# Kernel optimization log

Hardware: AMD Instinct MI355X
Metric: run time of the kernel (lower is better)

## Reference

```python
import jax, jax.numpy as jnp
import numpy as np

N_ROUTINGS = 3


def squash(v, axis=-1):
    sn = jnp.sum(jnp.square(v), axis=axis, keepdims=True)
    return (jnp.sqrt(sn) / (1.0 + sn)) * v


def setup_inputs() -> dict:
    key = jax.random.key(0)
    k1, k2 = jax.random.split(key)
    B, R, C, n_in, d_in = 16, 14, 14, 64, 16
    n_caps, caps_dim = 10, 16
    inputs = jax.random.normal(k1, (B, R, C, n_in, d_in), dtype=jnp.float32)
    W = jax.random.normal(k2, (n_caps, n_in, d_in, caps_dim), dtype=jnp.float32) * 0.1
    return {"inputs": inputs, "W": W}


def reference(inputs, W):
    # inputs: [B,R,C,i,e], W: [n,i,e,o] -> res (u_hat): [B,R,C,n,i,o]
    res = jnp.einsum('brcie,nieo->brcnio', inputs, W)
    n_in = inputs.shape[3]
    # softmax of zeros over last axis -> uniform 1/n_in
    b = jnp.full(res.shape[:-1], 1.0 / n_in, dtype=res.dtype)  # [B,R,C,n,i]
    for _ in range(N_ROUTINGS - 1):
        v = squash(jnp.sum(b[..., None] * res, axis=-2))  # [B,R,C,n,o]
        b = b + jnp.sum(res * v[..., None, :], axis=-1)   # agreement
    out = squash(jnp.sum(b[..., None] * res, axis=-2))
    return out  # [B,R,C,n_caps,caps_dim]
```

## Files before the change

kernel.cpp:

```cpp
#include <hip/hip_runtime.h>
#include <hip/hip_bf16.h>

typedef __attribute__((ext_vector_type(4))) float f32x4;
typedef __attribute__((ext_vector_type(8))) short s16x8;

#define QPB 4


template<int CTRL>
__device__ __forceinline__ float dpp_add(float x) {
    int v = __builtin_amdgcn_update_dpp(0, __float_as_int(x), CTRL, 0xF, 0xF, true);
    return x + __int_as_float(v);
}
template<int CTRL>
__device__ __forceinline__ float dpp_movf(float x) {
    return __int_as_float(__builtin_amdgcn_update_dpp(0, __float_as_int(x), CTRL, 0xF, 0xF, true));
}

__global__ __launch_bounds__(256, 4) void caps_kernel(
    const float* __restrict__ inp,
    const float* __restrict__ W,
    float* __restrict__ out)
{
    const int tid = threadIdx.x;
    const int w   = tid >> 6;
    const int l   = tid & 63;
    const int n   = blockIdx.x / 196;
    const int qg  = blockIdx.x % 196;
    const int q0  = qg * QPB;

    extern __shared__ __align__(16) char smem[];
    char* res_s = smem;

    const int i4 = l >> 2;
    const int oq = l & 3;
    const int i_ = w * 16 + i4;
    const int col = l & 15;
    const int kg  = l >> 4;

    const float* wb = W + (size_t)n * 16384 + i_ * 256 + oq * 4;
    f32x4 wrot[16];
#pragma unroll
    for (int r = 0; r < 4; ++r) {
        int c = (oq + r) & 3;
#pragma unroll
        for (int kk = 0; kk < 4; ++kk)
            wrot[r * 4 + kk] = *(const f32x4*)(wb + (c * 4 + kk) * 16);
    }

    s16x8 ones;
#pragma unroll
    for (int j = 0; j < 8; ++j) ones[j] = (short)0x3F80;

    for (int t = 0; t < QPB; ++t) {
        const int q = q0 + t;
        char* rbuf = res_s + (t & 1) * 8192;

        f32x4 raw[4];
#pragma unroll
        for (int p = 0; p < 4; ++p)
            raw[p] = *(const f32x4*)(inp + (size_t)q * 4096 + p * 1024 + w * 256 + l * 4);

#pragma unroll
        for (int p = 0; p < 4; ++p) {
            f32x4 a = raw[p];
            f32x4 acc = (f32x4)0.0f;
#pragma unroll
            for (int kk = 0; kk < 4; ++kk) acc += a[kk] * wrot[kk];
            f32x4 b1;
#pragma unroll
            for (int kk = 0; kk < 4; ++kk) b1[kk] = dpp_movf<0x39>(a[kk]);
#pragma unroll
            for (int kk = 0; kk < 4; ++kk) acc += b1[kk] * wrot[4 + kk];
            f32x4 b2;
#pragma unroll
            for (int kk = 0; kk < 4; ++kk) b2[kk] = dpp_movf<0x4E>(a[kk]);
#pragma unroll
            for (int kk = 0; kk < 4; ++kk) acc += b2[kk] * wrot[8 + kk];
            f32x4 b3;
#pragma unroll
            for (int kk = 0; kk < 4; ++kk) b3[kk] = dpp_movf<0x93>(a[kk]);
#pragma unroll
            for (int kk = 0; kk < 4; ++kk) acc += b3[kk] * wrot[12 + kk];

#pragma unroll
            for (int dd = 0; dd < 4; ++dd) {
                int o = oq * 4 + dd;
                __hip_bfloat16 bb = __float2bfloat16(acc[dd]);
                int byte = p * 2048 + o * 128 + (((i_ >> 3) ^ (o & 7)) << 4) + (i_ & 7) * 2;
                *(unsigned short*)(rbuf + byte) = *(unsigned short*)&bb;
            }
        }

        asm volatile("s_waitcnt lgkmcnt(0)" ::: "memory");
        __builtin_amdgcn_s_barrier();
        asm volatile("" ::: "memory");
        __builtin_amdgcn_sched_barrier(0);

        s16x8 fr0 = *(const s16x8*)(rbuf + w * 2048 + col * 128 + (((kg + 0) ^ (col & 7)) << 4));
        s16x8 fr1 = *(const s16x8*)(rbuf + w * 2048 + col * 128 + (((kg + 4) ^ (col & 7)) << 4));

        f32x4 G  = (f32x4)0.0f;
        f32x4 C2 = (f32x4)0.0f;
        G  = __builtin_amdgcn_mfma_f32_16x16x32_bf16(fr0, fr0, G, 0, 0, 0);
        G  = __builtin_amdgcn_mfma_f32_16x16x32_bf16(fr1, fr1, G, 0, 0, 0);
        C2 = __builtin_amdgcn_mfma_f32_16x16x32_bf16(ones, fr0, C2, 0, 0, 0);
        C2 = __builtin_amdgcn_mfma_f32_16x16x32_bf16(ones, fr1, C2, 0, 0, 0);

        float s = C2[0] * (1.0f / 64.0f);

#pragma unroll
        for (int it = 0; it < 2; ++it) {
            float sn = s * s;
            sn = dpp_add<0xB1>(sn);
            sn = dpp_add<0x4E>(sn);
            sn = dpp_add<0x124>(sn);
            sn = dpp_add<0x128>(sn);
            float scale = sqrtf(sn) / (1.0f + sn);
            float v = scale * s;
            float v0 = __shfl(v, kg * 4 + 0);
            float v1 = __shfl(v, kg * 4 + 1);
            float v2 = __shfl(v, kg * 4 + 2);
            float v3 = __shfl(v, kg * 4 + 3);
            float acc = G[0] * v0 + G[1] * v1 + G[2] * v2 + G[3] * v3;
            acc += __shfl_xor(acc, 16);
            acc += __shfl_xor(acc, 32);
            s += acc;
        }

        float sn = s * s;
        sn = dpp_add<0xB1>(sn);
        sn = dpp_add<0x4E>(sn);
        sn = dpp_add<0x124>(sn);
        sn = dpp_add<0x128>(sn);
        float scale = sqrtf(sn) / (1.0f + sn);
        float v = scale * s;

        if (l < 16)
            out[((size_t)(q * 4 + w) * 10 + n) * 16 + col] = v;
    }
}

extern "C" void kernel_launch(void* const* d_in, const int* in_sizes, int n_in,
                              void* d_out, int out_size, void* d_ws, size_t ws_size,
                              hipStream_t stream) {
    const float* inp = (const float*)d_in[0];
    const float* W   = (const float*)d_in[1];
    float* out = (float*)d_out;

    dim3 grid(1960), block(256);
    hipLaunchKernelGGL(caps_kernel, grid, block, 16384, stream, inp, W, out);
}
```

Measured before the change: 34.42 us.

## Process two positions per phase and prefetch next pair's inputs during compute

Result: faster. 31.65 us (-8.0%).

```diff
diff --git a/kernel.cpp b/kernel.cpp
--- a/kernel.cpp
+++ b/kernel.cpp
@@ -3,8 +3,6 @@
 
 typedef __attribute__((ext_vector_type(4))) float f32x4;
 typedef __attribute__((ext_vector_type(8))) short s16x8;
-
-#define QPB 4
 
 
 template<int CTRL>
@@ -17,7 +15,7 @@
     return __int_as_float(__builtin_amdgcn_update_dpp(0, __float_as_int(x), CTRL, 0xF, 0xF, true));
 }
 
-__global__ __launch_bounds__(256, 4) void caps_kernel(
+__global__ __launch_bounds__(256, 3) void caps_kernel(
     const float* __restrict__ inp,
     const float* __restrict__ W,
     float* __restrict__ out)
@@ -27,7 +25,7 @@
     const int l   = tid & 63;
     const int n   = blockIdx.x / 196;
     const int qg  = blockIdx.x % 196;
-    const int q0  = qg * QPB;
+    const int q0  = qg * 4;
 
     extern __shared__ __align__(16) char smem[];
     char* res_s = smem;
@@ -52,18 +50,19 @@
 #pragma unroll
     for (int j = 0; j < 8; ++j) ones[j] = (short)0x3F80;
 
-    for (int t = 0; t < QPB; ++t) {
-        const int q = q0 + t;
-        char* rbuf = res_s + (t & 1) * 8192;
-
-        f32x4 raw[4];
+    f32x4 raw[8];
 #pragma unroll
-        for (int p = 0; p < 4; ++p)
-            raw[p] = *(const f32x4*)(inp + (size_t)q * 4096 + p * 1024 + w * 256 + l * 4);
+    for (int pp = 0; pp < 8; ++pp)
+        raw[pp] = *(const f32x4*)(inp + (size_t)q0 * 4096 + pp * 1024 + w * 256 + l * 4);
 
 #pragma unroll
-        for (int p = 0; p < 4; ++p) {
-            f32x4 a = raw[p];
+    for (int t = 0; t < 2; ++t) {
+        char* rbuf = res_s + (t & 1) * 16384;
+        const int qb = q0 + 2 * t;
+
+#pragma unroll
+        for (int pp = 0; pp < 8; ++pp) {
+            f32x4 a = raw[pp];
             f32x4 acc = (f32x4)0.0f;
 #pragma unroll
             for (int kk = 0; kk < 4; ++kk) acc += a[kk] * wrot[kk];
@@ -87,9 +86,15 @@
             for (int dd = 0; dd < 4; ++dd) {
                 int o = oq * 4 + dd;
                 __hip_bfloat16 bb = __float2bfloat16(acc[dd]);
-                int byte = p * 2048 + o * 128 + (((i_ >> 3) ^ (o & 7)) << 4) + (i_ & 7) * 2;
+                int byte = pp * 2048 + o * 128 + (((i_ >> 3) ^ (o & 7)) << 4) + (i_ & 7) * 2;
                 *(unsigned short*)(rbuf + byte) = *(unsigned short*)&bb;
             }
+        }
+
+        if (t == 0) {
+#pragma unroll
+            for (int pp = 0; pp < 8; ++pp)
+                raw[pp] = *(const f32x4*)(inp + (size_t)(q0 + 2) * 4096 + pp * 1024 + w * 256 + l * 4);
         }
 
         asm volatile("s_waitcnt lgkmcnt(0)" ::: "memory");
@@ -97,47 +102,57 @@
         asm volatile("" ::: "memory");
         __builtin_amdgcn_sched_barrier(0);
 
-        s16x8 fr0 = *(const s16x8*)(rbuf + w * 2048 + col * 128 + (((kg + 0) ^ (col & 7)) << 4));
-        s16x8 fr1 = *(const s16x8*)(rbuf + w * 2048 + col * 128 + (((kg + 4) ^ (col & 7)) << 4));
-
-        f32x4 G  = (f32x4)0.0f;
-        f32x4 C2 = (f32x4)0.0f;
-        G  = __builtin_amdgcn_mfma_f32_16x16x32_bf16(fr0, fr0, G, 0, 0, 0);
-        G  = __builtin_amdgcn_mfma_f32_16x16x32_bf16(fr1, fr1, G, 0, 0, 0);
-        C2 = __builtin_amdgcn_mfma_f32_16x16x32_bf16(ones, fr0, C2, 0, 0, 0);
-        C2 = __builtin_amdgcn_mfma_f32_16x16x32_bf16(ones, fr1, C2, 0, 0, 0);
-
-        float s = C2[0] * (1.0f / 64.0f);
+        float s[2];
+        f32x4 G[2];
+#pragma unroll
+        for (int c = 0; c < 2; ++c) {
+            const int pp = w + 4 * c;
+            s16x8 fr0 = *(const s16x8*)(rbuf + pp * 2048 + col * 128 + (((kg + 0) ^ (col & 7)) << 4));
+            s16x8 fr1 = *(const s16x8*)(rbuf + pp * 2048 + col * 128 + (((kg + 4) ^ (col & 7)) << 4));
+            f32x4 g  = (f32x4)0.0f;
+            f32x4 c2 = (f32x4)0.0f;
+            g  = __builtin_amdgcn_mfma_f32_16x16x32_bf16(fr0, fr0, g, 0, 0, 0);
+            g  = __builtin_amdgcn_mfma_f32_16x16x32_bf16(fr1, fr1, g, 0, 0, 0);
+            c2 = __builtin_amdgcn_mfma_f32_16x16x32_bf16(ones, fr0, c2, 0, 0, 0);
+            c2 = __builtin_amdgcn_mfma_f32_16x16x32_bf16(ones, fr1, c2, 0, 0, 0);
+            G[c] = g;
+            s[c] = c2[0] * (1.0f / 64.0f);
+        }
 
 #pragma unroll
         for (int it = 0; it < 2; ++it) {
-            float sn = s * s;
+#pragma unroll
+            for (int c = 0; c < 2; ++c) {
+                float sn = s[c] * s[c];
+                sn = dpp_add<0xB1>(sn);
+                sn = dpp_add<0x4E>(sn);
+                sn = dpp_add<0x124>(sn);
+                sn = dpp_add<0x128>(sn);
+                float scale = sqrtf(sn) / (1.0f + sn);
+                float v = scale * s[c];
+                float v0 = __shfl(v, kg * 4 + 0);
+                float v1 = __shfl(v, kg * 4 + 1);
+                float v2 = __shfl(v, kg * 4 + 2);
+                float v3 = __shfl(v, kg * 4 + 3);
+                float acc = G[c][0] * v0 + G[c][1] * v1 + G[c][2] * v2 + G[c][3] * v3;
+                acc += __shfl_xor(acc, 16);
+                acc += __shfl_xor(acc, 32);
+                s[c] += acc;
+            }
+        }
+
+#pragma unroll
+        for (int c = 0; c < 2; ++c) {
+            float sn = s[c] * s[c];
             sn = dpp_add<0xB1>(sn);
             sn = dpp_add<0x4E>(sn);
             sn = dpp_add<0x124>(sn);
             sn = dpp_add<0x128>(sn);
             float scale = sqrtf(sn) / (1.0f + sn);
-            float v = scale * s;
-            float v0 = __shfl(v, kg * 4 + 0);
-            float v1 = __shfl(v, kg * 4 + 1);
-            float v2 = __shfl(v, kg * 4 + 2);
-            float v3 = __shfl(v, kg * 4 + 3);
-            float acc = G[0] * v0 + G[1] * v1 + G[2] * v2 + G[3] * v3;
-            acc += __shfl_xor(acc, 16);
-            acc += __shfl_xor(acc, 32);
-            s += acc;
+            float v = scale * s[c];
+            if (l < 16)
+                out[((size_t)((qb + c) * 4 + w) * 10 + n) * 16 + col] = v;
         }
-
-        float sn = s * s;
-        sn = dpp_add<0xB1>(sn);
-        sn = dpp_add<0x4E>(sn);
-        sn = dpp_add<0x124>(sn);
-        sn = dpp_add<0x128>(sn);
-        float scale = sqrtf(sn) / (1.0f + sn);
-        float v = scale * s;
-
-        if (l < 16)
-            out[((size_t)(q * 4 + w) * 10 + n) * 16 + col] = v;
     }
 }
 
@@ -149,5 +164,5 @@
     float* out = (float*)d_out;
 
     dim3 grid(1960), block(256);
-    hipLaunchKernelGGL(caps_kernel, grid, block, 16384, stream, inp, W, out);
+    hipLaunchKernelGGL(caps_kernel, grid, block, 32768, stream, inp, W, out);
 }
```
